# Kernel optimization log

Measured on AMD Instinct MI355X. Metric: run time of the kernel, lower is better.

The kernel has to match this reference:

```python
import jax, jax.numpy as jnp
import numpy as np
from jax import lax

B, DKV, L = 2048, 64, 128   # batch, in/out channels (d_k==d_v), seq len (== d_model)
H, DT = 16, 32              # n_head, d_trans
KW, PAD = 13, 6             # conv kernel width / padding
EPS = 1e-3                  # LayerNormalization eps
TEMPER = np.float32(np.sqrt(128.0))  # sqrt(d_model)


def conv1d(x, w, b):
    # x: (B, Cin, L), w: (Cout, Cin, KW) -> (B, Cout, L)
    y = lax.conv_general_dilated(x, w, window_strides=(1,), padding=[(PAD, PAD)],
                                 dimension_numbers=('NCH', 'OIH', 'NCH'))
    return y + b[None, :, None]


def setup_inputs() -> dict:
    key = jax.random.key(0)
    ks = jax.random.split(key, 20)
    n = lambda i, shape, s: jax.random.normal(ks[i], shape, dtype=jnp.float32) * s
    return {
        'q': n(0, (B, DKV, L), 1.0),
        'k': n(1, (B, DKV, L), 1.0),
        'v': n(2, (B, DKV, L), 1.0),
        # conv projections c_q/c_k/c_v: Conv1d(d_k or d_v -> d_trans, kernel 13)
        'cq_w': n(3, (DT, DKV, KW), 0.05), 'cq_b': n(4, (DT,), 0.05),
        'ck_w': n(5, (DT, DKV, KW), 0.05), 'ck_b': n(6, (DT,), 0.05),
        'cv_w': n(7, (DT, DKV, KW), 0.05), 'cv_b': n(8, (DT,), 0.05),
        # per-head projections (n_head, d_model=128, d_trans=32), xavier-ish scale
        'w_qs': n(9, (H, L, DT), 0.08), 'w_ks': n(10, (H, L, DT), 0.08), 'w_vs': n(11, (H, L, DT), 0.08),
        # proj: Linear(n_head*d_trans=512 -> d_model=128)
        'proj_w': n(12, (L, H * DT), 0.05), 'proj_b': n(13, (L,), 0.05),
        # final_conv: Conv1d(d_trans=32 -> d_v=64, kernel 13)
        'fc_w': n(14, (DKV, DT, KW), 0.05), 'fc_b': n(15, (DKV,), 0.05),
        # custom LayerNormalization over last dim (size 128)
        'ln_a': jnp.ones((L,), jnp.float32), 'ln_b': jnp.zeros((L,), jnp.float32),
    }


def reference(q, k, v, cq_w, cq_b, ck_w, ck_b, cv_w, cv_b,
              w_qs, w_ks, w_vs, proj_w, proj_b, fc_w, fc_b, ln_a, ln_b):
    residual = q  # (B, DKV, L)
    qb = conv1d(q, cq_w, cq_b)  # (B, DT, L)
    kb = conv1d(k, ck_w, ck_b)
    vb = conv1d(v, cv_w, cv_b)
    # per-head linear maps along the length-128 axis: (B,DT,L) x (H,L,DT) -> (H,B,DT,DT)
    qh = jnp.einsum('btl,hld->hbtd', qb, w_qs)
    kh = jnp.einsum('btl,hld->hbtd', kb, w_ks)
    vh = jnp.einsum('btl,hld->hbtd', vb, w_vs)
    scores = jnp.einsum('hbqd,hbkd->hbqk', qh, kh) / TEMPER  # (H,B,32,32)
    attn = jax.nn.softmax(scores, axis=-1)  # dropout inactive at eval
    out = jnp.einsum('hbqk,hbkd->hbqd', attn, vh)  # (H,B,32,32)
    # torch.cat(split(...,B,0), -1) concatenates heads along features, head-major
    out = out.transpose(1, 2, 0, 3).reshape(B, DT, H * DT)  # (B,32,512)
    out = out @ proj_w.T + proj_b  # (B,32,128)
    out = conv1d(out, fc_w, fc_b)  # (B,64,128)
    z = out + residual
    # custom LayerNormalization: unbiased std, divide by (std + eps)
    mu = jnp.mean(z, axis=-1, keepdims=True)
    sigma = jnp.sqrt(jnp.sum((z - mu) ** 2, axis=-1, keepdims=True) / (L - 1))
    return (z - mu) / (sigma + EPS) * ln_a + ln_b
```

## Files before the change

### kernel.cpp

```cpp
#include <hip/hip_runtime.h>
#include <math.h>

#define DEV_INLINE __device__ __forceinline__

constexpr int NB = 2048;
constexpr int C  = 64;
constexpr int L  = 128;
constexpr int DT = 32;
constexpr int NH = 16;
constexpr int KW = 13;
constexpr int PADC = 6;
constexpr float LN_EPS = 1e-3f;
constexpr float RTEMPER = 0.08838834764831845f;

using frag_ab = __attribute__((ext_vector_type(8))) short;
using frag_cd = __attribute__((ext_vector_type(4))) float;

union alignas(16) F16x8 { short s[8]; short4 h[2]; frag_ab f; };

DEV_INLINE short f2bf(float x) {
    unsigned u = __float_as_uint(x);
    unsigned r = (u + 0x7FFFu + ((u >> 16) & 1u)) >> 16;
    return (short)r;
}
DEV_INLINE unsigned pack2bf(float a, float b) {
    return (unsigned)(unsigned short)f2bf(a) | ((unsigned)(unsigned short)f2bf(b) << 16);
}

__global__ __launch_bounds__(256) void k0_prep(
    const float* __restrict__ wqs, const float* __restrict__ wks,
    const float* __restrict__ wvs, const float* __restrict__ pw,
    const float* __restrict__ cqw, const float* __restrict__ ckw,
    const float* __restrict__ cvw, const float* __restrict__ fcw,
    short* __restrict__ wqB, short* __restrict__ wkB, short* __restrict__ wvB,
    short* __restrict__ projB,
    short* __restrict__ cqA, short* __restrict__ ckA, short* __restrict__ cvA,
    short* __restrict__ fcA)
{
    int idx = blockIdx.x * 256 + threadIdx.x;
    if (idx >= 46080) return;
    F16x8 u;
    if (idx < 32768) {
        int arr = idx >> 13;
        int rem = idx & 8191;
        int h   = rem >> 9;
        int f   = (rem >> 6) & 7;
        int ln  = rem & 63;
        if (arr < 3) {
            const float* w = (arr == 0) ? wqs : (arr == 1 ? wks : wvs);
            int kt = f >> 1, nt = f & 1;
            int n = nt * 16 + (ln & 15);
            int kb = kt * 32 + ((ln >> 4) << 3);
            #pragma unroll
            for (int j = 0; j < 8; ++j)
                u.s[j] = f2bf(w[h * 4096 + (kb + j) * 32 + n]);
            short* dst = (arr == 0) ? wqB : (arr == 1 ? wkB : wvB);
            *(F16x8*)(dst + rem * 8) = u;
        } else {
            int m = f * 16 + (ln & 15);
            int db = (ln >> 4) << 3;
            #pragma unroll
            for (int j = 0; j < 8; ++j)
                u.s[j] = f2bf(pw[m * 512 + h * 32 + db + j]);
            *(F16x8*)(projB + rem * 8) = u;
        }
    } else {
        int idx2 = idx - 32768;
        int arr2 = idx2 / 3328;
        int rem2 = idx2 - arr2 * 3328;
        int f  = rem2 >> 6;
        int ln = rem2 & 63;
        int q8 = (ln >> 4) << 3;
        if (arr2 < 3) {
            const float* w = (arr2 == 0) ? cqw : (arr2 == 1 ? ckw : cvw);
            int mt = f & 1, kt = (f >> 1) & 1, kw = f >> 2;
            int m = mt * 16 + (ln & 15);
            int cib = kt * 32 + q8;
            #pragma unroll
            for (int j = 0; j < 8; ++j)
                u.s[j] = f2bf(w[m * (C * KW) + (cib + j) * KW + kw]);
            short* dst = (arr2 == 0) ? cqA : (arr2 == 1 ? ckA : cvA);
            *(F16x8*)(dst + rem2 * 8) = u;
        } else {
            int mt = f & 3, kw = f >> 2;
            int m = mt * 16 + (ln & 15);
            #pragma unroll
            for (int j = 0; j < 8; ++j)
                u.s[j] = f2bf(fcw[m * (DT * KW) + (q8 + j) * KW + kw]);
            *(F16x8*)(fcA + rem2 * 8) = u;
        }
    }
}

DEV_INLINE frag_ab ld_frag(const short* buf, int rbase, int lane) {
    const short* p = buf + (rbase + (lane & 15)) * 36 + ((lane >> 4) << 3);
    F16x8 u;
    u.h[0] = *(const short4*)p;
    u.h[1] = *(const short4*)(p + 4);
    return u.f;
}
DEV_INLINE void st_cfrag(short* buf, frag_cd c, int mt, int nt, int lane) {
    const int col = nt * 16 + (lane & 15);
    const int r0  = mt * 16 + ((lane >> 4) << 2);
    #pragma unroll
    for (int i = 0; i < 4; ++i) buf[(r0 + i) * 36 + col] = f2bf(c[i]);
}
DEV_INLINE void st_cfragT(short* buf, frag_cd c, int mt, int nt, int lane) {
    const int col = nt * 16 + (lane & 15);
    const int r0  = mt * 16 + ((lane >> 4) << 2);
    #pragma unroll
    for (int i = 0; i < 4; ++i) buf[col * 36 + r0 + i] = f2bf(c[i]);
}

DEV_INLINE void proj_head(const short* __restrict__ tile, const short* __restrict__ bF,
                          short* dst, bool transp, int lane) {
    frag_ab B[8];
    #pragma unroll
    for (int i = 0; i < 8; ++i)
        B[i] = *(const frag_ab*)(bF + (i * 64 + lane) * 8);
    #pragma unroll
    for (int mt = 0; mt < 2; ++mt) {
        frag_ab A[4];
        #pragma unroll
        for (int kt = 0; kt < 4; ++kt) {
            const short* p = tile + (mt * 16 + (lane & 15)) * 136 + kt * 32 + ((lane >> 4) << 3);
            F16x8 u; u.h[0] = *(const short4*)p; u.h[1] = *(const short4*)(p + 4);
            A[kt] = u.f;
        }
        #pragma unroll
        for (int nt = 0; nt < 2; ++nt) {
            frag_cd acc = {0.f, 0.f, 0.f, 0.f};
            #pragma unroll
            for (int kt = 0; kt < 4; ++kt)
                acc = __builtin_amdgcn_mfma_f32_16x16x32_bf16(A[kt], B[kt*2+nt], acc, 0, 0, 0);
            if (transp) st_cfragT(dst, acc, mt, nt, lane);
            else        st_cfrag (dst, acc, mt, nt, lane);
        }
    }
}

__global__ __launch_bounds__(256, 3) void k_fused(
    const float* __restrict__ qx, const float* __restrict__ kx, const float* __restrict__ vx,
    const short* __restrict__ cqA, const short* __restrict__ ckA, const short* __restrict__ cvA,
    const float* __restrict__ cqb, const float* __restrict__ ckb, const float* __restrict__ cvb,
    const short* __restrict__ wqB, const short* __restrict__ wkB, const short* __restrict__ wvB,
    const short* __restrict__ projB, const float* __restrict__ proj_b,
    const short* __restrict__ fA, const float* __restrict__ fcb,
    const float* __restrict__ ln_a, const float* __restrict__ ln_b,
    float* __restrict__ out)
{
    __shared__ __align__(16) char smem[53760];
    short* tiles = (short*)smem;
    short* regB  = (short*)(smem + 26112);

    const int b = blockIdx.x, tid = threadIdx.x;
    const int lane = tid & 63, wv = tid >> 6;
    const int qq = lane >> 4, nlo = lane & 15;
    const int nb0 = wv * 32 + nlo;

    {
        const float* xs[3] = { qx + (size_t)b * 8192, kx + (size_t)b * 8192, vx + (size_t)b * 8192 };
        const short* was[3] = { cqA, ckA, cvA };
        const float* bss[3] = { cqb, ckb, cvb };
        short* xT = regB;
        #pragma unroll
        for (int inp = 0; inp < 3; ++inp) {
            const float* xb = xs[inp];
            for (int i = tid; i < 1024; i += 256) {
                int cp = i >> 5, l4 = (i & 31) << 2;
                float4 a  = *(const float4*)(xb + (2 * cp) * 128 + l4);
                float4 c2 = *(const float4*)(xb + (2 * cp + 1) * 128 + l4);
                *(unsigned*)&xT[(l4 + 6) * 72 + 2 * cp] = pack2bf(a.x, c2.x);
                *(unsigned*)&xT[(l4 + 7) * 72 + 2 * cp] = pack2bf(a.y, c2.y);
                *(unsigned*)&xT[(l4 + 8) * 72 + 2 * cp] = pack2bf(a.z, c2.z);
                *(unsigned*)&xT[(l4 + 9) * 72 + 2 * cp] = pack2bf(a.w, c2.w);
            }
            for (int i = tid; i < 384; i += 256) {
                int rr = i >> 5, c2i = (i & 31) * 2;
                int r = rr < 6 ? rr : 128 + rr;
                *(unsigned*)&xT[r * 72 + c2i] = 0u;
            }

            frag_cd acc[2][2];
            const float* bias = bss[inp];
            #pragma unroll
            for (int mt = 0; mt < 2; ++mt)
                #pragma unroll
                for (int i = 0; i < 4; ++i) {
                    float bv = bias[mt * 16 + qq * 4 + i];
                    acc[mt][0][i] = bv; acc[mt][1][i] = bv;
                }
            __syncthreads();

            const short* wA = was[inp];
            for (int f = 0; f < 26; ++f) {
                const int kw = f >> 1;
                frag_ab a0 = *(const frag_ab*)(wA + ((f * 2 + 0) * 64 + lane) * 8);
                frag_ab a1 = *(const frag_ab*)(wA + ((f * 2 + 1) * 64 + lane) * 8);
                const short* bp = &xT[(nb0 + kw) * 72 + (f & 1) * 32 + qq * 8];
                frag_ab b0 = *(const frag_ab*)bp;
                frag_ab b1 = *(const frag_ab*)(bp + 16 * 72);
                acc[0][0] = __builtin_amdgcn_mfma_f32_16x16x32_bf16(a0, b0, acc[0][0], 0, 0, 0);
                acc[0][1] = __builtin_amdgcn_mfma_f32_16x16x32_bf16(a0, b1, acc[0][1], 0, 0, 0);
                acc[1][0] = __builtin_amdgcn_mfma_f32_16x16x32_bf16(a1, b0, acc[1][0], 0, 0, 0);
                acc[1][1] = __builtin_amdgcn_mfma_f32_16x16x32_bf16(a1, b1, acc[1][1], 0, 0, 0);
            }

            short* dstTile = tiles + inp * 4352;
            #pragma unroll
            for (int mt = 0; mt < 2; ++mt)
                #pragma unroll
                for (int ntl = 0; ntl < 2; ++ntl) {
                    int col = wv * 32 + ntl * 16 + nlo;
                    int r0  = mt * 16 + qq * 4;
                    #pragma unroll
                    for (int i = 0; i < 4; ++i)
                        dstTile[(r0 + i) * 136 + col] = f2bf(acc[mt][ntl][i]);
                }
            __syncthreads();
        }
    }

    short* buf0 = regB + wv * 3456;
    short* buf1 = buf0 + 1152;
    short* buf2 = buf1 + 1152;

    frag_cd oc[2][2];
    #pragma unroll
    for (int mt = 0; mt < 2; ++mt)
        #pragma unroll
        for (int nt = 0; nt < 2; ++nt)
            oc[mt][nt] = frag_cd{0.f, 0.f, 0.f, 0.f};

    for (int r = 0; r < 4; ++r) {
        const int h = r * 4 + wv;
        proj_head(tiles,        wqB + h * 4096, buf0, false, lane);
        proj_head(tiles + 4352, wkB + h * 4096, buf1, false, lane);
        proj_head(tiles + 8704, wvB + h * 4096, buf2, true,  lane);

        frag_ab bk0 = ld_frag(buf1, 0, lane), bk1 = ld_frag(buf1, 16, lane);
        frag_cd S[2][2];
        #pragma unroll
        for (int mt = 0; mt < 2; ++mt) {
            frag_ab aq = ld_frag(buf0, mt * 16, lane);
            frag_cd z = {0.f, 0.f, 0.f, 0.f};
            S[mt][0] = __builtin_amdgcn_mfma_f32_16x16x32_bf16(aq, bk0, z, 0, 0, 0);
            S[mt][1] = __builtin_amdgcn_mfma_f32_16x16x32_bf16(aq, bk1, z, 0, 0, 0);
        }

        #pragma unroll
        for (int mt = 0; mt < 2; ++mt) {
            #pragma unroll
            for (int i = 0; i < 4; ++i) {
                float s0 = S[mt][0][i] * RTEMPER;
                float s1 = S[mt][1][i] * RTEMPER;
                float mx = fmaxf(s0, s1);
                #pragma unroll
                for (int off = 1; off < 16; off <<= 1)
                    mx = fmaxf(mx, __shfl_xor(mx, off, 64));
                float e0 = __expf(s0 - mx), e1 = __expf(s1 - mx);
                float sm = e0 + e1;
                #pragma unroll
                for (int off = 1; off < 16; off <<= 1)
                    sm += __shfl_xor(sm, off, 64);
                const float inv = 1.f / sm;
                const int row = mt * 16 + ((lane >> 4) << 2) + i;
                buf0[row * 36 + (lane & 15)]      = f2bf(e0 * inv);
                buf0[row * 36 + 16 + (lane & 15)] = f2bf(e1 * inv);
            }
        }

        frag_ab bv0 = ld_frag(buf2, 0, lane), bv1 = ld_frag(buf2, 16, lane);
        #pragma unroll
        for (int mt = 0; mt < 2; ++mt) {
            frag_ab ap = ld_frag(buf0, mt * 16, lane);
            frag_cd z = {0.f, 0.f, 0.f, 0.f};
            frag_cd O0 = __builtin_amdgcn_mfma_f32_16x16x32_bf16(ap, bv0, z, 0, 0, 0);
            frag_cd O1 = __builtin_amdgcn_mfma_f32_16x16x32_bf16(ap, bv1, z, 0, 0, 0);
            st_cfrag(buf1, O0, mt, 0, lane);
            st_cfrag(buf1, O1, mt, 1, lane);
        }
        __syncthreads();

        #pragma unroll
        for (int hh = 0; hh < 4; ++hh) {
            const short* ob = regB + hh * 3456 + 1152;
            frag_ab ao0 = ld_frag(ob, 0, lane), ao1 = ld_frag(ob, 16, lane);
            const int hq = r * 4 + hh;
            #pragma unroll
            for (int nt = 0; nt < 2; ++nt) {
                frag_ab pb = *(const frag_ab*)(projB + hq * 4096 + ((wv * 2 + nt) * 64 + lane) * 8);
                oc[0][nt] = __builtin_amdgcn_mfma_f32_16x16x32_bf16(ao0, pb, oc[0][nt], 0, 0, 0);
                oc[1][nt] = __builtin_amdgcn_mfma_f32_16x16x32_bf16(ao1, pb, oc[1][nt], 0, 0, 0);
            }
        }
        __syncthreads();
    }

    short* xT2 = tiles;
    for (int i = tid; i < 384; i += 256) {
        int rr = i >> 5, cc = i & 31;
        int rw = rr < 6 ? rr : 128 + rr;
        xT2[rw * 40 + cc] = 0;
    }
    {
        const float pbv0 = proj_b[wv * 32 + (lane & 15)];
        const float pbv1 = proj_b[wv * 32 + 16 + (lane & 15)];
        #pragma unroll
        for (int mt = 0; mt < 2; ++mt)
            #pragma unroll
            for (int nt = 0; nt < 2; ++nt) {
                const int l = wv * 32 + nt * 16 + (lane & 15);
                const float pbv = nt ? pbv1 : pbv0;
                #pragma unroll
                for (int i = 0; i < 4; ++i) {
                    const int t = mt * 16 + ((lane >> 4) << 2) + i;
                    xT2[(l + 6) * 40 + t] = f2bf(oc[mt][nt][i] + pbv);
                }
            }
    }
    __syncthreads();

    frag_cd fa[4][2];
    #pragma unroll
    for (int mt = 0; mt < 4; ++mt)
        #pragma unroll
        for (int i = 0; i < 4; ++i) {
            float bv = fcb[mt * 16 + qq * 4 + i];
            fa[mt][0][i] = bv; fa[mt][1][i] = bv;
        }
    for (int kw = 0; kw < 13; ++kw) {
        frag_ab a[4];
        #pragma unroll
        for (int mt = 0; mt < 4; ++mt)
            a[mt] = *(const frag_ab*)(fA + ((kw * 4 + mt) * 64 + lane) * 8);
        const short* bp = &xT2[(nb0 + kw) * 40 + qq * 8];
        frag_ab b0 = *(const frag_ab*)bp;
        frag_ab b1 = *(const frag_ab*)(bp + 16 * 40);
        #pragma unroll
        for (int mt = 0; mt < 4; ++mt) {
            fa[mt][0] = __builtin_amdgcn_mfma_f32_16x16x32_bf16(a[mt], b0, fa[mt][0], 0, 0, 0);
            fa[mt][1] = __builtin_amdgcn_mfma_f32_16x16x32_bf16(a[mt], b1, fa[mt][1], 0, 0, 0);
        }
    }
    __syncthreads();

    float* zb = (float*)smem;
    #pragma unroll
    for (int mt = 0; mt < 4; ++mt)
        #pragma unroll
        for (int ntl = 0; ntl < 2; ++ntl) {
            int col = wv * 32 + ntl * 16 + nlo;
            int r0  = mt * 16 + qq * 4;
            #pragma unroll
            for (int i = 0; i < 4; ++i)
                zb[(r0 + i) * 132 + col] = fa[mt][ntl][i];
        }
    __syncthreads();

    const int cq2 = tid >> 4, lq = tid & 15, l0 = lq * 8;
    const float4* la4 = (const float4*)(ln_a + l0);
    const float4* lb4 = (const float4*)(ln_b + l0);
    float4 A0 = la4[0], A1 = la4[1], B0 = lb4[0], B1 = lb4[1];
    for (int g = 0; g < 4; ++g) {
        const int co = g * 16 + cq2;
        const float4* zr4 = (const float4*)(&zb[co * 132 + l0]);
        float4 z0 = zr4[0], z1 = zr4[1];
        const float4* rr4 = (const float4*)(qx + (size_t)b * (C * L) + co * 128 + l0);
        float4 r0 = rr4[0], r1 = rr4[1];
        float zz[8] = {z0.x + r0.x, z0.y + r0.y, z0.z + r0.z, z0.w + r0.w,
                       z1.x + r1.x, z1.y + r1.y, z1.z + r1.z, z1.w + r1.w};
        float s = 0.f;
        #pragma unroll
        for (int j = 0; j < 8; ++j) s += zz[j];
        #pragma unroll
        for (int off = 1; off < 16; off <<= 1) s += __shfl_xor(s, off, 64);
        const float mu = s * (1.f / 128.f);
        float d[8], ss = 0.f;
        #pragma unroll
        for (int j = 0; j < 8; ++j) { d[j] = zz[j] - mu; ss += d[j] * d[j]; }
        #pragma unroll
        for (int off = 1; off < 16; off <<= 1) ss += __shfl_xor(ss, off, 64);
        const float sigma = sqrtf(ss * (1.f / 127.f));
        const float inv = 1.f / (sigma + LN_EPS);
        float4 o0, o1;
        o0.x = fmaf(d[0] * inv, A0.x, B0.x);
        o0.y = fmaf(d[1] * inv, A0.y, B0.y);
        o0.z = fmaf(d[2] * inv, A0.z, B0.z);
        o0.w = fmaf(d[3] * inv, A0.w, B0.w);
        o1.x = fmaf(d[4] * inv, A1.x, B1.x);
        o1.y = fmaf(d[5] * inv, A1.y, B1.y);
        o1.z = fmaf(d[6] * inv, A1.z, B1.z);
        o1.w = fmaf(d[7] * inv, A1.w, B1.w);
        float4* ow = (float4*)(out + (size_t)b * (C * L) + co * 128 + l0);
        ow[0] = o0; ow[1] = o1;
    }
}

extern "C" void kernel_launch(void* const* d_in, const int* in_sizes, int n_in,
                              void* d_out, int out_size, void* d_ws, size_t ws_size,
                              hipStream_t stream) {
    const float* q    = (const float*)d_in[0];
    const float* k    = (const float*)d_in[1];
    const float* v    = (const float*)d_in[2];
    const float* cq_w = (const float*)d_in[3];  const float* cq_b = (const float*)d_in[4];
    const float* ck_w = (const float*)d_in[5];  const float* ck_b = (const float*)d_in[6];
    const float* cv_w = (const float*)d_in[7];  const float* cv_b = (const float*)d_in[8];
    const float* w_qs = (const float*)d_in[9];
    const float* w_ks = (const float*)d_in[10];
    const float* w_vs = (const float*)d_in[11];
    const float* proj_w = (const float*)d_in[12];
    const float* proj_b = (const float*)d_in[13];
    const float* fc_w = (const float*)d_in[14]; const float* fc_b = (const float*)d_in[15];
    const float* ln_a = (const float*)d_in[16]; const float* ln_b = (const float*)d_in[17];
    float* out = (float*)d_out;

    short* ws16 = (short*)d_ws;
    short* wqB = ws16;
    short* wkB = wqB + 65536;
    short* wvB = wkB + 65536;
    short* projB = wvB + 65536;
    short* cqA = projB + 65536;
    short* ckA = cqA + 26624;
    short* cvA = ckA + 26624;
    short* fcA = cvA + 26624;

    k0_prep<<<180, 256, 0, stream>>>(w_qs, w_ks, w_vs, proj_w,
                                     cq_w, ck_w, cv_w, fc_w,
                                     wqB, wkB, wvB, projB, cqA, ckA, cvA, fcA);
    k_fused<<<NB, 256, 0, stream>>>(q, k, v, cqA, ckA, cvA, cq_b, ck_b, cv_b,
                                    wqB, wkB, wvB, projB, proj_b,
                                    fcA, fc_b, ln_a, ln_b, out);
}
```

Measured before the change: 379.7 us.

## Shrink and swizzle LDS buffers to raise fused-kernel occupancy to four blocks

```diff
diff --git a/kernel.cpp b/kernel.cpp
--- a/kernel.cpp
+++ b/kernel.cpp
@@ -23,8 +23,15 @@
     unsigned r = (u + 0x7FFFu + ((u >> 16) & 1u)) >> 16;
     return (short)r;
 }
-DEV_INLINE unsigned pack2bf(float a, float b) {
-    return (unsigned)(unsigned short)f2bf(a) | ((unsigned)(unsigned short)f2bf(b) << 16);
+
+DEV_INLINE int tswz(int r, int c) {
+    int g = (r ^ (r >> 3)) & 7;
+    int blk = c >> 3;
+    return r * 128 + ((((blk & 8) | ((blk ^ g) & 7))) << 3) + (c & 7);
+}
+DEV_INLINE int bswz(int r, int c) {
+    int f = (r ^ (r >> 2)) & 3;
+    return r * 32 + ((((c >> 3) ^ f) & 3) << 3) + (c & 7);
 }
 
 __global__ __launch_bounds__(256) void k0_prep(
@@ -93,23 +100,20 @@
 }
 
 DEV_INLINE frag_ab ld_frag(const short* buf, int rbase, int lane) {
-    const short* p = buf + (rbase + (lane & 15)) * 36 + ((lane >> 4) << 3);
-    F16x8 u;
-    u.h[0] = *(const short4*)p;
-    u.h[1] = *(const short4*)(p + 4);
-    return u.f;
+    return *(const frag_ab*)(buf + bswz(rbase + (lane & 15), (lane >> 4) << 3));
 }
 DEV_INLINE void st_cfrag(short* buf, frag_cd c, int mt, int nt, int lane) {
     const int col = nt * 16 + (lane & 15);
     const int r0  = mt * 16 + ((lane >> 4) << 2);
     #pragma unroll
-    for (int i = 0; i < 4; ++i) buf[(r0 + i) * 36 + col] = f2bf(c[i]);
+    for (int i = 0; i < 4; ++i) buf[bswz(r0 + i, col)] = f2bf(c[i]);
 }
 DEV_INLINE void st_cfragT(short* buf, frag_cd c, int mt, int nt, int lane) {
-    const int col = nt * 16 + (lane & 15);
-    const int r0  = mt * 16 + ((lane >> 4) << 2);
-    #pragma unroll
-    for (int i = 0; i < 4; ++i) buf[col * 36 + r0 + i] = f2bf(c[i]);
+    const int row = nt * 16 + (lane & 15);
+    const int c0  = mt * 16 + ((lane >> 4) << 2);
+    short4 s4;
+    s4.x = f2bf(c[0]); s4.y = f2bf(c[1]); s4.z = f2bf(c[2]); s4.w = f2bf(c[3]);
+    *(short4*)(buf + bswz(row, c0)) = s4;
 }
 
 DEV_INLINE void proj_head(const short* __restrict__ tile, const short* __restrict__ bF,
@@ -122,11 +126,9 @@
     for (int mt = 0; mt < 2; ++mt) {
         frag_ab A[4];
         #pragma unroll
-        for (int kt = 0; kt < 4; ++kt) {
-            const short* p = tile + (mt * 16 + (lane & 15)) * 136 + kt * 32 + ((lane >> 4) << 3);
-            F16x8 u; u.h[0] = *(const short4*)p; u.h[1] = *(const short4*)(p + 4);
-            A[kt] = u.f;
-        }
+        for (int kt = 0; kt < 4; ++kt)
+            A[kt] = *(const frag_ab*)(tile +
+                        tswz(mt * 16 + (lane & 15), kt * 32 + ((lane >> 4) << 3)));
         #pragma unroll
         for (int nt = 0; nt < 2; ++nt) {
             frag_cd acc = {0.f, 0.f, 0.f, 0.f};
@@ -139,7 +141,7 @@
     }
 }
 
-__global__ __launch_bounds__(256, 3) void k_fused(
+__global__ __launch_bounds__(256, 4) void k_fused(
     const float* __restrict__ qx, const float* __restrict__ kx, const float* __restrict__ vx,
     const short* __restrict__ cqA, const short* __restrict__ ckA, const short* __restrict__ cvA,
     const float* __restrict__ cqb, const float* __restrict__ ckb, const float* __restrict__ cvb,
@@ -149,37 +151,41 @@
     const float* __restrict__ ln_a, const float* __restrict__ ln_b,
     float* __restrict__ out)
 {
-    __shared__ __align__(16) char smem[53760];
-    short* tiles = (short*)smem;
-    short* regB  = (short*)(smem + 26112);
+    __shared__ __align__(16) char smem[40960];
+    short* S16   = (short*)smem;
+    short* tiles = S16;
+    short* xT    = S16 + 8192;
+    short* bufs  = S16 + 12288;
 
     const int b = blockIdx.x, tid = threadIdx.x;
     const int lane = tid & 63, wv = tid >> 6;
     const int qq = lane >> 4, nlo = lane & 15;
     const int nb0 = wv * 32 + nlo;
 
+    if (tid < 96) {
+        int rr = tid >> 3, c0 = (tid & 7) * 8;
+        int rw = rr < 6 ? rr : 128 + rr;
+        F16x8 z;
+        #pragma unroll
+        for (int j = 0; j < 8; ++j) z.s[j] = 0;
+        *(F16x8*)(xT + rw * 72 + c0) = z;
+    }
     {
         const float* xs[3] = { qx + (size_t)b * 8192, kx + (size_t)b * 8192, vx + (size_t)b * 8192 };
         const short* was[3] = { cqA, ckA, cvA };
         const float* bss[3] = { cqb, ckb, cvb };
-        short* xT = regB;
         #pragma unroll
         for (int inp = 0; inp < 3; ++inp) {
             const float* xb = xs[inp];
             for (int i = tid; i < 1024; i += 256) {
-                int cp = i >> 5, l4 = (i & 31) << 2;
-                float4 a  = *(const float4*)(xb + (2 * cp) * 128 + l4);
-                float4 c2 = *(const float4*)(xb + (2 * cp + 1) * 128 + l4);
-                *(unsigned*)&xT[(l4 + 6) * 72 + 2 * cp] = pack2bf(a.x, c2.x);
-                *(unsigned*)&xT[(l4 + 7) * 72 + 2 * cp] = pack2bf(a.y, c2.y);
-                *(unsigned*)&xT[(l4 + 8) * 72 + 2 * cp] = pack2bf(a.z, c2.z);
-                *(unsigned*)&xT[(l4 + 9) * 72 + 2 * cp] = pack2bf(a.w, c2.w);
+                int l = i & 127, c0 = i >> 7;
+                const float* px = xb + c0 * 1024 + l;
+                F16x8 u;
+                #pragma unroll
+                for (int j = 0; j < 8; ++j) u.s[j] = f2bf(px[j * 128]);
+                *(F16x8*)(xT + (l + 6) * 72 + c0 * 8) = u;
             }
-            for (int i = tid; i < 384; i += 256) {
-                int rr = i >> 5, c2i = (i & 31) * 2;
-                int r = rr < 6 ? rr : 128 + rr;
-                *(unsigned*)&xT[r * 72 + c2i] = 0u;
-            }
+            __syncthreads();
 
             frag_cd acc[2][2];
             const float* bias = bss[inp];
@@ -190,7 +196,6 @@
                     float bv = bias[mt * 16 + qq * 4 + i];
                     acc[mt][0][i] = bv; acc[mt][1][i] = bv;
                 }
-            __syncthreads();
 
             const short* wA = was[inp];
             for (int f = 0; f < 26; ++f) {
@@ -205,8 +210,9 @@
                 acc[1][0] = __builtin_amdgcn_mfma_f32_16x16x32_bf16(a1, b0, acc[1][0], 0, 0, 0);
                 acc[1][1] = __builtin_amdgcn_mfma_f32_16x16x32_bf16(a1, b1, acc[1][1], 0, 0, 0);
             }
-
-            short* dstTile = tiles + inp * 4352;
+            __syncthreads();
+
+            short* dstT = tiles + inp * 4096;
             #pragma unroll
             for (int mt = 0; mt < 2; ++mt)
                 #pragma unroll
@@ -215,15 +221,14 @@
                     int r0  = mt * 16 + qq * 4;
                     #pragma unroll
                     for (int i = 0; i < 4; ++i)
-                        dstTile[(r0 + i) * 136 + col] = f2bf(acc[mt][ntl][i]);
+                        dstT[tswz(r0 + i, col)] = f2bf(acc[mt][ntl][i]);
                 }
-            __syncthreads();
-        }
-    }
-
-    short* buf0 = regB + wv * 3456;
-    short* buf1 = buf0 + 1152;
-    short* buf2 = buf1 + 1152;
+        }
+    }
+    __syncthreads();
+
+    short* bufA = bufs + wv * 2048;
+    short* bufB = bufA + 1024;
 
     frag_cd oc[2][2];
     #pragma unroll
@@ -234,19 +239,21 @@
 
     for (int r = 0; r < 4; ++r) {
         const int h = r * 4 + wv;
-        proj_head(tiles,        wqB + h * 4096, buf0, false, lane);
-        proj_head(tiles + 4352, wkB + h * 4096, buf1, false, lane);
-        proj_head(tiles + 8704, wvB + h * 4096, buf2, true,  lane);
-
-        frag_ab bk0 = ld_frag(buf1, 0, lane), bk1 = ld_frag(buf1, 16, lane);
+        proj_head(tiles,        wqB + h * 4096, bufA, false, lane);
+        proj_head(tiles + 4096, wkB + h * 4096, bufB, false, lane);
+
+        frag_ab bk0 = ld_frag(bufB, 0, lane), bk1 = ld_frag(bufB, 16, lane);
+        frag_ab aq0 = ld_frag(bufA, 0, lane), aq1 = ld_frag(bufA, 16, lane);
         frag_cd S[2][2];
-        #pragma unroll
-        for (int mt = 0; mt < 2; ++mt) {
-            frag_ab aq = ld_frag(buf0, mt * 16, lane);
+        {
             frag_cd z = {0.f, 0.f, 0.f, 0.f};
-            S[mt][0] = __builtin_amdgcn_mfma_f32_16x16x32_bf16(aq, bk0, z, 0, 0, 0);
-            S[mt][1] = __builtin_amdgcn_mfma_f32_16x16x32_bf16(aq, bk1, z, 0, 0, 0);
-        }
+            S[0][0] = __builtin_amdgcn_mfma_f32_16x16x32_bf16(aq0, bk0, z, 0, 0, 0);
+            S[0][1] = __builtin_amdgcn_mfma_f32_16x16x32_bf16(aq0, bk1, z, 0, 0, 0);
+            S[1][0] = __builtin_amdgcn_mfma_f32_16x16x32_bf16(aq1, bk0, z, 0, 0, 0);
+            S[1][1] = __builtin_amdgcn_mfma_f32_16x16x32_bf16(aq1, bk1, z, 0, 0, 0);
+        }
+
+        proj_head(tiles + 8192, wvB + h * 4096, bufB, true, lane);
 
         #pragma unroll
         for (int mt = 0; mt < 2; ++mt) {
@@ -265,26 +272,30 @@
                     sm += __shfl_xor(sm, off, 64);
                 const float inv = 1.f / sm;
                 const int row = mt * 16 + ((lane >> 4) << 2) + i;
-                buf0[row * 36 + (lane & 15)]      = f2bf(e0 * inv);
-                buf0[row * 36 + 16 + (lane & 15)] = f2bf(e1 * inv);
+                bufA[bswz(row, nlo)]      = f2bf(e0 * inv);
+                bufA[bswz(row, 16 + nlo)] = f2bf(e1 * inv);
             }
         }
 
-        frag_ab bv0 = ld_frag(buf2, 0, lane), bv1 = ld_frag(buf2, 16, lane);
-        #pragma unroll
-        for (int mt = 0; mt < 2; ++mt) {
-            frag_ab ap = ld_frag(buf0, mt * 16, lane);
+        frag_ab bv0 = ld_frag(bufB, 0, lane), bv1 = ld_frag(bufB, 16, lane);
+        frag_ab ap0 = ld_frag(bufA, 0, lane), ap1 = ld_frag(bufA, 16, lane);
+        frag_cd O00, O01, O10, O11;
+        {
             frag_cd z = {0.f, 0.f, 0.f, 0.f};
-            frag_cd O0 = __builtin_amdgcn_mfma_f32_16x16x32_bf16(ap, bv0, z, 0, 0, 0);
-            frag_cd O1 = __builtin_amdgcn_mfma_f32_16x16x32_bf16(ap, bv1, z, 0, 0, 0);
-            st_cfrag(buf1, O0, mt, 0, lane);
-            st_cfrag(buf1, O1, mt, 1, lane);
-        }
+            O00 = __builtin_amdgcn_mfma_f32_16x16x32_bf16(ap0, bv0, z, 0, 0, 0);
+            O01 = __builtin_amdgcn_mfma_f32_16x16x32_bf16(ap0, bv1, z, 0, 0, 0);
+            O10 = __builtin_amdgcn_mfma_f32_16x16x32_bf16(ap1, bv0, z, 0, 0, 0);
+            O11 = __builtin_amdgcn_mfma_f32_16x16x32_bf16(ap1, bv1, z, 0, 0, 0);
+        }
+        st_cfrag(bufA, O00, 0, 0, lane);
+        st_cfrag(bufA, O01, 0, 1, lane);
+        st_cfrag(bufA, O10, 1, 0, lane);
+        st_cfrag(bufA, O11, 1, 1, lane);
         __syncthreads();
 
         #pragma unroll
         for (int hh = 0; hh < 4; ++hh) {
-            const short* ob = regB + hh * 3456 + 1152;
+            const short* ob = bufs + hh * 2048;
             frag_ab ao0 = ld_frag(ob, 0, lane), ao1 = ld_frag(ob, 16, lane);
             const int hq = r * 4 + hh;
             #pragma unroll
@@ -297,11 +308,12 @@
         __syncthreads();
     }
 
-    short* xT2 = tiles;
-    for (int i = tid; i < 384; i += 256) {
-        int rr = i >> 5, cc = i & 31;
+    short* xT2 = S16;
+    if (tid < 96) {
+        int rr = tid >> 3, c4 = (tid & 7) * 4;
         int rw = rr < 6 ? rr : 128 + rr;
-        xT2[rw * 40 + cc] = 0;
+        short4 z; z.x = z.y = z.z = z.w = 0;
+        *(short4*)(xT2 + rw * 40 + c4) = z;
     }
     {
         const float pbv0 = proj_b[wv * 32 + (lane & 15)];
@@ -312,11 +324,12 @@
             for (int nt = 0; nt < 2; ++nt) {
                 const int l = wv * 32 + nt * 16 + (lane & 15);
                 const float pbv = nt ? pbv1 : pbv0;
-                #pragma unroll
-                for (int i = 0; i < 4; ++i) {
-                    const int t = mt * 16 + ((lane >> 4) << 2) + i;
-                    xT2[(l + 6) * 40 + t] = f2bf(oc[mt][nt][i] + pbv);
-                }
+                short4 s4;
+                s4.x = f2bf(oc[mt][nt][0] + pbv);
+                s4.y = f2bf(oc[mt][nt][1] + pbv);
+                s4.z = f2bf(oc[mt][nt][2] + pbv);
+                s4.w = f2bf(oc[mt][nt][3] + pbv);
+                *(short4*)(xT2 + (l + 6) * 40 + mt * 16 + qq * 4) = s4;
             }
     }
     __syncthreads();
```

New measurement: 432.8 us. +14.0%, slower.
